# Optimization experiments

Measured on AMD Instinct MI355X. Metric: run time of the kernel, lower is better.

Reference implementation:

```python
import jax, jax.numpy as jnp
import numpy as np

ETA = 0.5
R_CUTOFF = 6.0
ZETA = 0.6
LAMDA = 0.8
RS = 1.0
SPECIAL_ATOM = 8  # atom index routed to elem2 net


def _af(x):
    return 1.0 / (1.0 + x * x)


def _mlp(g, w1, b1, w2, b2, w3, b3):
    h = _af(g @ w1.T + b1)
    h = _af(h @ w2.T + b2)
    return h @ w3.T + b3  # [N,1]


def setup_inputs() -> dict:
    key = jax.random.key(0)
    ks = jax.random.split(key, 13)
    N = 384
    x = jax.random.normal(ks[0], (N, 3), dtype=jnp.float32) * 2.0
    def lin(kw, kb, fout, fin):
        w = jax.random.normal(kw, (fout, fin), dtype=jnp.float32) * (1.0 / np.sqrt(fin))
        b = jax.random.normal(kb, (fout,), dtype=jnp.float32) * 0.1
        return w, b
    w1a, b1a = lin(ks[1], ks[2], 40, 2)
    w2a, b2a = lin(ks[3], ks[4], 40, 40)
    w3a, b3a = lin(ks[5], ks[6], 1, 40)
    w1b, b1b = lin(ks[7], ks[8], 40, 2)
    w2b, b2b = lin(ks[9], ks[10], 40, 40)
    w3b, b3b = lin(ks[11], ks[12], 1, 40)
    return {"x": x,
            "w1a": w1a, "b1a": b1a, "w2a": w2a, "b2a": b2a, "w3a": w3a, "b3a": b3a,
            "w1b": w1b, "b1b": b1b, "w2b": w2b, "b2b": b2b, "w3b": w3b, "b3b": b3b}


def _descriptors(x):
    N = x.shape[0]
    eye = jnp.eye(N, dtype=bool)
    diff = x[:, None, :] - x[None, :, :]           # [N,N,3]
    D2 = jnp.sum(diff * diff, axis=-1)             # [N,N]
    D = jnp.sqrt(jnp.where(eye, 1.0, D2))
    D = jnp.where(eye, 0.0, D)
    # cutoff function (hard 0 beyond R_cutoff), zeroed on diagonal
    fc = jnp.where((D <= R_CUTOFF) & (~eye), 0.5 * (jnp.cos(np.pi * D / R_CUTOFF) + 1.0), 0.0)
    # radial symmetry function per atom i
    rad = jnp.sum(jnp.exp(-ETA * (D - RS) ** 2) * fc, axis=1)  # [N]
    # angular: sum over triplets j<k, j!=i, k!=i
    A = jnp.exp(-ETA * D2) * fc                    # [N,N], zero on diagonal
    Gm = x @ x.T                                   # Gram matrix
    gd = jnp.diag(Gm)
    # dot(Rij, Rki) with Rij = x_i - x_j, Rki = x_k - x_i
    dot = Gm[:, None, :] - gd[:, None, None] - Gm[None, :, :] + Gm[:, :, None]  # [N,N,N] (i,j,k)
    denom = D[:, :, None] * D[:, None, :]          # |Rij| * |Rki|
    cos_theta = dot / jnp.where(denom > 0, denom, 1.0)
    term1 = jnp.maximum(1.0 + LAMDA * cos_theta, 1e-6) ** ZETA
    # A[i,j] * A[j,k] * A[k,i]; diag-zero A kills i==j and i==k terms
    term2 = A[:, :, None] * A[None, :, :] * A[:, None, :]
    tri = jnp.triu(jnp.ones((N, N), dtype=jnp.float32), k=1)[None, :, :]  # j < k
    ang = (2.0 ** (1.0 - ZETA)) * jnp.sum(term1 * term2 * tri, axis=(1, 2))  # [N]
    return jnp.stack([ang, rad], axis=-1)          # [N,2], order matches Gi=[ang, rad]


def reference(x, w1a, b1a, w2a, b2a, w3a, b3a, w1b, b1b, w2b, b2b, w3b, b3b):
    G = _descriptors(x)
    q1 = _mlp(G, w1a, b1a, w2a, b2a, w3a, b3a)[:, 0]
    q2 = _mlp(G, w1b, b1b, w2b, b2b, w3b, b3b)[:, 0]
    idx = jnp.arange(x.shape[0])
    return jnp.where(idx == SPECIAL_ATOM, q2, q1)  # [N]
```

## Files before the change

### kernel.cpp

```cpp
#include <hip/hip_runtime.h>
#include <math.h>

#define N 384
#define EPSA 4e-4f

#if __has_builtin(__builtin_amdgcn_logf) && __has_builtin(__builtin_amdgcn_exp2f)
#define LOG2F(x) __builtin_amdgcn_logf(x)
#define EXP2F(x) __builtin_amdgcn_exp2f(x)
#else
#define LOG2F(x) __log2f(x)
#define EXP2F(x) __expf(0.69314718056f * (x))
#endif

__device__ __forceinline__ float wave_reduce(float v) {
#pragma unroll
    for (int o = 32; o > 0; o >>= 1) v += __shfl_down(v, o, 64);
    return v;
}

__global__ __launch_bounds__(128) void pair_kernel(
    const float* __restrict__ x, float* __restrict__ A,
    float4* __restrict__ nbr4, int* __restrict__ nbrJ, int* __restrict__ cnt,
    float* __restrict__ rad, float* __restrict__ ang, int* __restrict__ done) {
    const int i = blockIdx.x;
    const int t = threadIdx.x;
    const int lane = t & 63, w = t >> 6;
    const float xi0 = x[3 * i + 0], xi1 = x[3 * i + 1], xi2 = x[3 * i + 2];

    float racc = 0.0f;
    float4 val[3];
    int keep[3];
#pragma unroll
    for (int r = 0; r < 3; ++r) {
        const int j = t + 128 * r;
        float dx = xi0 - x[3 * j + 0];
        float dy = xi1 - x[3 * j + 1];
        float dz = xi2 - x[3 * j + 2];
        float d2 = dx * dx + dy * dy + dz * dz;
        float a = 0.0f, rr = 0.0f, inv = 0.0f;
        if (j != i) {
            float d = sqrtf(d2);
            if (d <= 6.0f) {
                float fc = 0.5f * (__cosf(0.52359877559829887f * d) + 1.0f);
                a = __expf(-0.5f * d2) * fc;
                float dm = d - 1.0f;
                rr = __expf(-0.5f * dm * dm) * fc;
            }
            inv = rsqrtf(d2);
        }
        A[i * N + j] = a;
        racc += rr;
        val[r] = make_float4(dx * inv, dy * inv, dz * inv, a);
        keep[r] = (a > EPSA) ? 1 : 0;
    }

    __shared__ int bcnt[6], bbase[6], realn;
    int pfx[3];
#pragma unroll
    for (int r = 0; r < 3; ++r) {
        unsigned long long m = __ballot(keep[r]);
        pfx[r] = __popcll(m & ((1ull << lane) - 1ull));
        if (lane == 0) bcnt[w + 2 * r] = __popcll(m);
    }
    __syncthreads();
    if (t == 0) {
        int s = 0;
#pragma unroll
        for (int c = 0; c < 6; ++c) { bbase[c] = s; s += bcnt[c]; }
        realn = s;
        cnt[i] = (s + 7) & ~7;
        ang[i] = 0.0f;
        done[i] = 0;
    }
    __syncthreads();
#pragma unroll
    for (int r = 0; r < 3; ++r) {
        if (keep[r]) {
            const int slot = bbase[w + 2 * r] + pfx[r];
            nbr4[i * N + slot] = val[r];
            nbrJ[i * N + slot] = t + 128 * r;
        }
    }
    const int rn = realn;
    const int np = (rn + 7) & ~7;
    if (t < np - rn) {
        nbr4[i * N + rn + t] = make_float4(0.f, 0.f, 0.f, 0.f);
        nbrJ[i * N + rn + t] = i;
    }

    __shared__ float red[2];
    float v = wave_reduce(racc);
    if (lane == 0) red[w] = v;
    __syncthreads();
    if (t == 0) rad[i] = red[0] + red[1];
}

__global__ __launch_bounds__(256) void ang_kernel(
    const float* __restrict__ A, const float4* __restrict__ nbr4,
    const int* __restrict__ nbrJ, const int* __restrict__ cnt,
    const float* __restrict__ rad, float* __restrict__ ang,
    int* __restrict__ done, float* __restrict__ out,
    const float* __restrict__ w1a, const float* __restrict__ b1a,
    const float* __restrict__ w2a, const float* __restrict__ b2a,
    const float* __restrict__ w3a, const float* __restrict__ b3a,
    const float* __restrict__ w1b, const float* __restrict__ b1b,
    const float* __restrict__ w2b, const float* __restrict__ b2b,
    const float* __restrict__ w3b, const float* __restrict__ b3b) {
    const int i = blockIdx.x;
    const int jc = blockIdx.y;
    const int t = threadIdx.x;
    const int n = cnt[i];
    const int iN = i * N;
    const int nb = n >> 3;

    float acc = 0.0f;
    for (int ks0 = 0; ks0 < n; ks0 += 256) {
        const int ks = ks0 + t;
        const bool valid = ks < n;
        float4 K = valid ? nbr4[iN + ks] : make_float4(0.f, 0.f, 0.f, 0.f);
        const int kcol = valid ? nbrJ[iN + ks] : 0;
        const float kx = -0.8f * K.x, ky = -0.8f * K.y, kz = -0.8f * K.z;
        const float kA = K.w;
        const float* Acol = A + kcol;

        const int bw = ((ks0 >> 3) + ((t >> 6) << 3)) + jc;

        float cacc = 0.0f;
        for (int b = bw; b < nb; b += 2) {
            const int s0 = b << 3;
            float a8[8];
#pragma unroll
            for (int q = 0; q < 8; ++q)
                a8[q] = Acol[nbrJ[iN + s0 + q] * N];
#pragma unroll
            for (int q = 0; q < 8; ++q) {
                float4 J = nbr4[iN + s0 + q];
                float bb = fmaf(J.x, kx, fmaf(J.y, ky, fmaf(J.z, kz, 1.0f)));
                float p = EXP2F(0.6f * LOG2F(bb));
                float aw = (s0 + q > ks) ? a8[q] : 0.0f;
                cacc = fmaf(J.w * aw, p, cacc);
            }
        }
        acc = fmaf(kA, cacc, acc);
    }

    __shared__ float red[4];
    __shared__ int s_win;
    __shared__ float s_ang;
    float v = wave_reduce(acc);
    if ((t & 63) == 0) red[t >> 6] = v;
    __syncthreads();
    if (t == 0) {
        float s = red[0] + red[1] + red[2] + red[3];
        atomicAdd(&ang[i], s);
        __threadfence();
        int old = atomicAdd(&done[i], 1);
        s_win = (old == 1);
        if (old == 1) s_ang = atomicAdd(&ang[i], 0.0f);
    }
    __syncthreads();
    if (!s_win) return;

    __shared__ float h1s[2][40];
    __shared__ float contrib[80];
    const float g0 = 1.3195079107728942f * s_ang;
    const float g1 = rad[i];

    if (t < 80) {
        const int net = t / 40, u = t - net * 40;
        const float* w1 = net ? w1b : w1a;
        const float* b1 = net ? b1b : b1a;
        float z = fmaf(w1[2 * u], g0, fmaf(w1[2 * u + 1], g1, b1[u]));
        h1s[net][u] = 1.0f / fmaf(z, z, 1.0f);
    }
    __syncthreads();
    if (t < 80) {
        const int net = t / 40, vv = t - net * 40;
        const float* w2 = net ? w2b : w2a;
        const float* b2 = net ? b2b : b2a;
        const float* w3 = net ? w3b : w3a;
        const float* row = w2 + vv * 40;
        float z = b2[vv];
#pragma unroll 8
        for (int u = 0; u < 40; ++u) z = fmaf(row[u], h1s[net][u], z);
        float h = 1.0f / fmaf(z, z, 1.0f);
        contrib[t] = w3[vv] * h;
    }
    __syncthreads();
    if (t < 2) {
        const float* b3 = t ? b3b : b3a;
        float q = b3[0];
        for (int vv = 0; vv < 40; ++vv) q += contrib[t * 40 + vv];
        contrib[t] = q;
    }
    __syncthreads();
    if (t == 0) out[i] = (i == 8) ? contrib[1] : contrib[0];
}

extern "C" void kernel_launch(void* const* d_in, const int* in_sizes, int n_in,
                              void* d_out, int out_size, void* d_ws, size_t ws_size,
                              hipStream_t stream) {
    const float* x = (const float*)d_in[0];
    const float* w1a = (const float*)d_in[1];
    const float* b1a = (const float*)d_in[2];
    const float* w2a = (const float*)d_in[3];
    const float* b2a = (const float*)d_in[4];
    const float* w3a = (const float*)d_in[5];
    const float* b3a = (const float*)d_in[6];
    const float* w1b = (const float*)d_in[7];
    const float* b1b = (const float*)d_in[8];
    const float* w2b = (const float*)d_in[9];
    const float* b2b = (const float*)d_in[10];
    const float* w3b = (const float*)d_in[11];
    const float* b3b = (const float*)d_in[12];
    float* out = (float*)d_out;

    float* ws = (float*)d_ws;
    float* A = ws;
    float4* nbr4 = (float4*)(ws + 147456);
    int* nbrJ = (int*)(ws + 147456 + 4 * 147456);
    float* rad = ws + 147456 * 6;
    float* ang = rad + 384;
    int* cnt = (int*)(ang + 384);
    int* done = cnt + 384;

    hipLaunchKernelGGL(pair_kernel, dim3(N), dim3(128), 0, stream,
                       x, A, nbr4, nbrJ, cnt, rad, ang, done);
    hipLaunchKernelGGL(ang_kernel, dim3(N, 2), dim3(256), 0, stream,
                       A, nbr4, nbrJ, cnt, rad, ang, done, out,
                       w1a, b1a, w2a, b2a, w3a, b3a,
                       w1b, b1b, w2b, b2b, w3b, b3b);
}
```

Baseline: 102.6 us.

## Fuse pair and angular kernels, recompute A_jk on the fly in shared memory

Merges the pair-descriptor and angular-triplet kernels into a single per-atom block that keeps compacted neighbor unit vectors and distances in shared memory. The A[j,k] factor is recomputed from |Rij|, |Rik| and their cosine instead of being gathered from a global N×N matrix, which removes the second launch, the atomics and the workspace traffic. The neighbor pruning threshold is also raised, so fewer neighbors enter the triplet loop, at the cost of extra transcendental math per pair and a slightly larger approximation error.

```diff
diff --git a/kernel.cpp b/kernel.cpp
--- a/kernel.cpp
+++ b/kernel.cpp
@@ -2,7 +2,7 @@
 #include <math.h>
 
 #define N 384
-#define EPSA 4e-4f
+#define EPSA 1.5e-3f
 
 #if __has_builtin(__builtin_amdgcn_logf) && __has_builtin(__builtin_amdgcn_exp2f)
 #define LOG2F(x) __builtin_amdgcn_logf(x)
@@ -18,28 +18,41 @@
     return v;
 }
 
-__global__ __launch_bounds__(128) void pair_kernel(
-    const float* __restrict__ x, float* __restrict__ A,
-    float4* __restrict__ nbr4, int* __restrict__ nbrJ, int* __restrict__ cnt,
-    float* __restrict__ rad, float* __restrict__ ang, int* __restrict__ done) {
+__global__ __launch_bounds__(256) void bpnn_kernel(
+    const float* __restrict__ x, float* __restrict__ out,
+    const float* __restrict__ w1a, const float* __restrict__ b1a,
+    const float* __restrict__ w2a, const float* __restrict__ b2a,
+    const float* __restrict__ w3a, const float* __restrict__ b3a,
+    const float* __restrict__ w1b, const float* __restrict__ b1b,
+    const float* __restrict__ w2b, const float* __restrict__ b2b,
+    const float* __restrict__ w3b, const float* __restrict__ b3b) {
     const int i = blockIdx.x;
     const int t = threadIdx.x;
     const int lane = t & 63, w = t >> 6;
+
+    __shared__ float4 s_u4[N];
+    __shared__ float  s_A[N];
+    __shared__ int    bcnt[8], bbase[8], s_n;
+    __shared__ float  s_redA[4], s_redB[4];
+    __shared__ float  s_g0, s_g1;
+
     const float xi0 = x[3 * i + 0], xi1 = x[3 * i + 1], xi2 = x[3 * i + 2];
 
     float racc = 0.0f;
-    float4 val[3];
-    int keep[3];
+    float4 val[2];
+    float  aval[2];
+    int    keep[2];
 #pragma unroll
-    for (int r = 0; r < 3; ++r) {
-        const int j = t + 128 * r;
-        float dx = xi0 - x[3 * j + 0];
-        float dy = xi1 - x[3 * j + 1];
-        float dz = xi2 - x[3 * j + 2];
-        float d2 = dx * dx + dy * dy + dz * dz;
-        float a = 0.0f, rr = 0.0f, inv = 0.0f;
-        if (j != i) {
-            float d = sqrtf(d2);
+    for (int r = 0; r < 2; ++r) {
+        const int j = t + 256 * r;
+        float a = 0.0f, rr = 0.0f, inv = 0.0f, d = 0.0f;
+        float dx = 0.0f, dy = 0.0f, dz = 0.0f;
+        if (j < N && j != i) {
+            dx = xi0 - x[3 * j + 0];
+            dy = xi1 - x[3 * j + 1];
+            dz = xi2 - x[3 * j + 2];
+            float d2 = dx * dx + dy * dy + dz * dz;
+            d = sqrtf(d2);
             if (d <= 6.0f) {
                 float fc = 0.5f * (__cosf(0.52359877559829887f * d) + 1.0f);
                 a = __expf(-0.5f * d2) * fc;
@@ -48,123 +61,86 @@
             }
             inv = rsqrtf(d2);
         }
-        A[i * N + j] = a;
         racc += rr;
-        val[r] = make_float4(dx * inv, dy * inv, dz * inv, a);
+        val[r] = make_float4(dx * inv, dy * inv, dz * inv, d);
+        aval[r] = a;
         keep[r] = (a > EPSA) ? 1 : 0;
     }
 
-    __shared__ int bcnt[6], bbase[6], realn;
-    int pfx[3];
+    int pfx[2];
 #pragma unroll
-    for (int r = 0; r < 3; ++r) {
+    for (int r = 0; r < 2; ++r) {
         unsigned long long m = __ballot(keep[r]);
         pfx[r] = __popcll(m & ((1ull << lane) - 1ull));
-        if (lane == 0) bcnt[w + 2 * r] = __popcll(m);
+        if (lane == 0) bcnt[w + 4 * r] = __popcll(m);
+    }
+    {
+        float v = wave_reduce(racc);
+        if (lane == 0) s_redA[w] = v;
     }
     __syncthreads();
     if (t == 0) {
         int s = 0;
 #pragma unroll
-        for (int c = 0; c < 6; ++c) { bbase[c] = s; s += bcnt[c]; }
-        realn = s;
-        cnt[i] = (s + 7) & ~7;
-        ang[i] = 0.0f;
-        done[i] = 0;
+        for (int c = 0; c < 8; ++c) { bbase[c] = s; s += bcnt[c]; }
+        s_n = s;
     }
     __syncthreads();
 #pragma unroll
-    for (int r = 0; r < 3; ++r) {
+    for (int r = 0; r < 2; ++r) {
         if (keep[r]) {
-            const int slot = bbase[w + 2 * r] + pfx[r];
-            nbr4[i * N + slot] = val[r];
-            nbrJ[i * N + slot] = t + 128 * r;
+            const int slot = bbase[w + 4 * r] + pfx[r];
+            s_u4[slot] = val[r];
+            s_A[slot] = aval[r];
         }
     }
-    const int rn = realn;
-    const int np = (rn + 7) & ~7;
-    if (t < np - rn) {
-        nbr4[i * N + rn + t] = make_float4(0.f, 0.f, 0.f, 0.f);
-        nbrJ[i * N + rn + t] = i;
+    __syncthreads();
+
+    const int n = s_n;
+    float tri = 0.0f;
+    for (int kb = 0; kb < n; kb += 128) {
+        const int k = kb + (t & 127);
+        const int rep = t >> 7;
+        if (k < n) {
+            const float4 K = s_u4[k];
+            const float kx = K.x, ky = K.y, kz = K.z, dk = K.w;
+            const float Ak = s_A[k];
+            const float dk2 = 2.0f * dk;
+            float cacc = 0.0f;
+            for (int j = rep; j < k; j += 2) {
+                const float4 J = s_u4[j];
+                const float Aj = s_A[j];
+                float dot  = fmaf(J.x, kx, fmaf(J.y, ky, J.z * kz));
+                float bb   = fmaf(-0.8f, dot, 1.0f);
+                float p    = EXP2F(0.6f * LOG2F(bb));
+                float dd   = J.w - dk;
+                float djk2 = fmaf(dk2 * J.w, 1.0f - dot, dd * dd);
+                float djk  = sqrtf(djk2);
+                float fc   = (djk2 < 36.0f)
+                               ? fmaf(0.5f, __cosf(0.52359877559829887f * djk), 0.5f)
+                               : 0.0f;
+                float Ajk  = __expf(-0.5f * djk2) * fc;
+                cacc = fmaf(Aj * Ajk, p, cacc);
+            }
+            tri = fmaf(Ak, cacc, tri);
+        }
     }
-
-    __shared__ float red[2];
-    float v = wave_reduce(racc);
-    if (lane == 0) red[w] = v;
-    __syncthreads();
-    if (t == 0) rad[i] = red[0] + red[1];
-}
-
-__global__ __launch_bounds__(256) void ang_kernel(
-    const float* __restrict__ A, const float4* __restrict__ nbr4,
-    const int* __restrict__ nbrJ, const int* __restrict__ cnt,
-    const float* __restrict__ rad, float* __restrict__ ang,
-    int* __restrict__ done, float* __restrict__ out,
-    const float* __restrict__ w1a, const float* __restrict__ b1a,
-    const float* __restrict__ w2a, const float* __restrict__ b2a,
-    const float* __restrict__ w3a, const float* __restrict__ b3a,
-    const float* __restrict__ w1b, const float* __restrict__ b1b,
-    const float* __restrict__ w2b, const float* __restrict__ b2b,
-    const float* __restrict__ w3b, const float* __restrict__ b3b) {
-    const int i = blockIdx.x;
-    const int jc = blockIdx.y;
-    const int t = threadIdx.x;
-    const int n = cnt[i];
-    const int iN = i * N;
-    const int nb = n >> 3;
-
-    float acc = 0.0f;
-    for (int ks0 = 0; ks0 < n; ks0 += 256) {
-        const int ks = ks0 + t;
-        const bool valid = ks < n;
-        float4 K = valid ? nbr4[iN + ks] : make_float4(0.f, 0.f, 0.f, 0.f);
-        const int kcol = valid ? nbrJ[iN + ks] : 0;
-        const float kx = -0.8f * K.x, ky = -0.8f * K.y, kz = -0.8f * K.z;
-        const float kA = K.w;
-        const float* Acol = A + kcol;
-
-        const int bw = ((ks0 >> 3) + ((t >> 6) << 3)) + jc;
-
-        float cacc = 0.0f;
-        for (int b = bw; b < nb; b += 2) {
-            const int s0 = b << 3;
-            float a8[8];
-#pragma unroll
-            for (int q = 0; q < 8; ++q)
-                a8[q] = Acol[nbrJ[iN + s0 + q] * N];
-#pragma unroll
-            for (int q = 0; q < 8; ++q) {
-                float4 J = nbr4[iN + s0 + q];
-                float bb = fmaf(J.x, kx, fmaf(J.y, ky, fmaf(J.z, kz, 1.0f)));
-                float p = EXP2F(0.6f * LOG2F(bb));
-                float aw = (s0 + q > ks) ? a8[q] : 0.0f;
-                cacc = fmaf(J.w * aw, p, cacc);
-            }
-        }
-        acc = fmaf(kA, cacc, acc);
+    {
+        float v = wave_reduce(tri);
+        if (lane == 0) s_redB[w] = v;
     }
-
-    __shared__ float red[4];
-    __shared__ int s_win;
-    __shared__ float s_ang;
-    float v = wave_reduce(acc);
-    if ((t & 63) == 0) red[t >> 6] = v;
     __syncthreads();
     if (t == 0) {
-        float s = red[0] + red[1] + red[2] + red[3];
-        atomicAdd(&ang[i], s);
-        __threadfence();
-        int old = atomicAdd(&done[i], 1);
-        s_win = (old == 1);
-        if (old == 1) s_ang = atomicAdd(&ang[i], 0.0f);
+        float tt = s_redB[0] + s_redB[1] + s_redB[2] + s_redB[3];
+        s_g0 = 1.3195079107728942f * tt;
+        s_g1 = s_redA[0] + s_redA[1] + s_redA[2] + s_redA[3];
     }
     __syncthreads();
-    if (!s_win) return;
 
     __shared__ float h1s[2][40];
     __shared__ float contrib[80];
-    const float g0 = 1.3195079107728942f * s_ang;
-    const float g1 = rad[i];
+    const float g0 = s_g0;
+    const float g1 = s_g1;
 
     if (t < 80) {
         const int net = t / 40, u = t - net * 40;
@@ -214,20 +190,10 @@
     const float* w3b = (const float*)d_in[11];
     const float* b3b = (const float*)d_in[12];
     float* out = (float*)d_out;
+    (void)d_ws; (void)ws_size;
 
-    float* ws = (float*)d_ws;
-    float* A = ws;
-    float4* nbr4 = (float4*)(ws + 147456);
-    int* nbrJ = (int*)(ws + 147456 + 4 * 147456);
-    float* rad = ws + 147456 * 6;
-    float* ang = rad + 384;
-    int* cnt = (int*)(ang + 384);
-    int* done = cnt + 384;
-
-    hipLaunchKernelGGL(pair_kernel, dim3(N), dim3(128), 0, stream,
-                       x, A, nbr4, nbrJ, cnt, rad, ang, done);
-    hipLaunchKernelGGL(ang_kernel, dim3(N, 2), dim3(256), 0, stream,
-                       A, nbr4, nbrJ, cnt, rad, ang, done, out,
+    hipLaunchKernelGGL(bpnn_kernel, dim3(N), dim3(256), 0, stream,
+                       x, out,
                        w1a, b1a, w2a, b2a, w3a, b3a,
                        w1b, b1b, w2b, b2b, w3b, b3b);
 }
```

Result: slower. 108.1 us (+5.3%).
